# Optimization experiments

Measured on AMD Instinct MI355X. Metric: run time of the kernel, lower is better.

Reference implementation:

```python
import jax, jax.numpy as jnp
import numpy as np
import math

L, B, S, D, H, DI, V = 4, 2, 1024, 768, 12, 3072, 512
DK = D // H

def gelu_tanh(x):
    c = math.sqrt(2.0 / math.pi)
    return 0.5 * x * (1.0 + jnp.tanh(c * (x + 0.044715 * x ** 3)))

def layer_norm(x, g, b, eps=1e-5):
    mu = jnp.mean(x, axis=-1, keepdims=True)
    var = jnp.var(x, axis=-1, keepdims=True)
    return (x - mu) * jax.lax.rsqrt(var + eps) * g + b

def setup_inputs() -> dict:
    key = jax.random.key(0)
    ks = jax.random.split(key, 12)
    w = 0.02  # init scale
    return {
        "x": jax.random.randint(ks[0], (B, S), 0, V),
        "embed": jax.random.normal(ks[1], (V, D), jnp.float32) * w,
        "pos_emb": jax.random.normal(ks[2], (S, D), jnp.float32) * w,
        "ln1_g": jnp.ones((L, D), jnp.float32),
        "ln1_b": jnp.zeros((L, D), jnp.float32),
        "wq": jax.random.normal(ks[3], (L, D, D), jnp.float32) * w,
        "bq": jnp.zeros((L, D), jnp.float32),
        "wk": jax.random.normal(ks[4], (L, D, D), jnp.float32) * w,
        "bk": jnp.zeros((L, D), jnp.float32),
        "wv": jax.random.normal(ks[5], (L, D, D), jnp.float32) * w,
        "bv": jnp.zeros((L, D), jnp.float32),
        "wo": jax.random.normal(ks[6], (L, D, D), jnp.float32) * w,
        "bo": jnp.zeros((L, D), jnp.float32),
        "ln2_g": jnp.ones((L, D), jnp.float32),
        "ln2_b": jnp.zeros((L, D), jnp.float32),
        "w_in": jax.random.normal(ks[7], (L, D, DI), jnp.float32) * w,
        "b_in": jnp.zeros((L, DI), jnp.float32),
        "w_out": jax.random.normal(ks[8], (L, DI, D), jnp.float32) * w,
        "b_out": jnp.zeros((L, D), jnp.float32),
        "lnf_g": jnp.ones((D,), jnp.float32),
        "lnf_b": jnp.zeros((D,), jnp.float32),
        "out_w": jax.random.normal(ks[9], (D, V), jnp.float32) * w,
    }

def reference(x, embed, pos_emb, ln1_g, ln1_b, wq, bq, wk, bk, wv, bv, wo, bo,
              ln2_g, ln2_b, w_in, b_in, w_out, b_out, lnf_g, lnf_b, out_w):
    s = x.shape[1]
    h = embed[x] + pos_emb[None, :s]                       # [B,S,D]
    causal = jnp.tril(jnp.ones((s, s), bool))              # True = keep
    scale = 1.0 / math.sqrt(DK)
    for l in range(L):
        a = layer_norm(h, ln1_g[l], ln1_b[l])
        q = (a @ wq[l] + bq[l]).reshape(-1, s, H, DK)
        k = (a @ wk[l] + bk[l]).reshape(-1, s, H, DK)
        v = (a @ wv[l] + bv[l]).reshape(-1, s, H, DK)
        scores = jnp.einsum('bqhd,bkhd->bhqk', q, k) * scale
        scores = jnp.where(causal, scores, -jnp.inf)
        attn = jax.nn.softmax(scores, axis=-1)
        o = jnp.einsum('bhqk,bkhd->bqhd', attn, v).reshape(-1, s, D)
        h = h + o @ wo[l] + bo[l]
        f = layer_norm(h, ln2_g[l], ln2_b[l])
        h = h + gelu_tanh(f @ w_in[l] + b_in[l]) @ w_out[l] + b_out[l]
    h = layer_norm(h, lnf_g, lnf_b)
    return h @ out_w                                       # [B,S,V] logits
```

## Files before the change

kernel.cpp:

```cpp
#include <hip/hip_runtime.h>
#include <hip/hip_bf16.h>


#define TKN    2048
#define DMODEL 768
#define SEQ    1024
#define NH     12
#define DHEAD  64
#define DFF    3072
#define NL     4
#define NVOCAB 512
#define NQKV   2304

typedef unsigned short u16;
typedef __attribute__((ext_vector_type(4))) float f32x4;
typedef __attribute__((ext_vector_type(8))) short short8;
typedef __attribute__((ext_vector_type(4))) unsigned short us4;

__device__ __forceinline__ u16 f2bf(float f) {
  unsigned u = __builtin_bit_cast(unsigned, f);
  u += 0x7fffu + ((u >> 16) & 1u);
  return (u16)(u >> 16);
}

__device__ __forceinline__ short8 mk8(us4 lo, us4 hi) {
  short8 r;
  r[0] = (short)lo[0]; r[1] = (short)lo[1]; r[2] = (short)lo[2]; r[3] = (short)lo[3];
  r[4] = (short)hi[0]; r[5] = (short)hi[1]; r[6] = (short)hi[2]; r[7] = (short)hi[3];
  return r;
}

__device__ __forceinline__ void gload16(const u16* g, u16* l) {
  __builtin_amdgcn_global_load_lds(
      (const __attribute__((address_space(1))) unsigned int*)g,
      (__attribute__((address_space(3))) unsigned int*)l, 16, 0, 0);
}

__global__ __launch_bounds__(256) void k_embed(const int* __restrict__ x,
                                               const float* __restrict__ emb,
                                               const float* __restrict__ pos,
                                               float* __restrict__ h) {
  int t = blockIdx.x;
  int s = t & (SEQ - 1);
  int id = x[t];
  int d = threadIdx.x;
#pragma unroll
  for (int j = 0; j < 3; ++j, d += 256)
    h[t * DMODEL + d] = emb[id * DMODEL + d] + pos[s * DMODEL + d];
}

__global__ __launch_bounds__(256) void k_ln(const float* __restrict__ h,
                                            const float* __restrict__ gam,
                                            const float* __restrict__ bet,
                                            u16* __restrict__ out) {
  __shared__ float sbuf[8];
  int row = blockIdx.x, tid = threadIdx.x;
  const float* hr = h + (size_t)row * DMODEL;
  float x0 = hr[tid], x1 = hr[tid + 256], x2 = hr[tid + 512];
  float s = x0 + x1 + x2;
#pragma unroll
  for (int off = 32; off > 0; off >>= 1) s += __shfl_down(s, off);
  if ((tid & 63) == 0) sbuf[tid >> 6] = s;
  __syncthreads();
  float mu = (sbuf[0] + sbuf[1] + sbuf[2] + sbuf[3]) * (1.0f / DMODEL);
  float d0 = x0 - mu, d1 = x1 - mu, d2 = x2 - mu;
  float v = d0 * d0 + d1 * d1 + d2 * d2;
#pragma unroll
  for (int off = 32; off > 0; off >>= 1) v += __shfl_down(v, off);
  if ((tid & 63) == 0) sbuf[4 + (tid >> 6)] = v;
  __syncthreads();
  float var = (sbuf[4] + sbuf[5] + sbuf[6] + sbuf[7]) * (1.0f / DMODEL);
  float rstd = rsqrtf(var + 1e-5f);
  size_t o = (size_t)row * DMODEL;
  out[o + tid]       = f2bf(d0 * rstd * gam[tid]       + bet[tid]);
  out[o + tid + 256] = f2bf(d1 * rstd * gam[tid + 256] + bet[tid + 256]);
  out[o + tid + 512] = f2bf(d2 * rstd * gam[tid + 512] + bet[tid + 512]);
}

__device__ __forceinline__ void cvt_tile(const float* __restrict__ src, int ldS,
                                         int k0, int n0src,
                                         u16* __restrict__ dst, int ldD, int n0dst,
                                         int tid, u16 (*tl)[72]) {
  int kr = tid >> 2, nj = (tid & 3) << 4;
  const float* sp = src + (size_t)(k0 + kr) * ldS + n0src + nj;
  float4 a0 = ((const float4*)sp)[0];
  float4 a1 = ((const float4*)sp)[1];
  float4 a2 = ((const float4*)sp)[2];
  float4 a3 = ((const float4*)sp)[3];
  u16* tr = &tl[kr][nj];
  tr[0]=f2bf(a0.x); tr[1]=f2bf(a0.y); tr[2]=f2bf(a0.z); tr[3]=f2bf(a0.w);
  tr[4]=f2bf(a1.x); tr[5]=f2bf(a1.y); tr[6]=f2bf(a1.z); tr[7]=f2bf(a1.w);
  tr[8]=f2bf(a2.x); tr[9]=f2bf(a2.y); tr[10]=f2bf(a2.z); tr[11]=f2bf(a2.w);
  tr[12]=f2bf(a3.x); tr[13]=f2bf(a3.y); tr[14]=f2bf(a3.z); tr[15]=f2bf(a3.w);
  __syncthreads();
  int nr = tid >> 2, kj = (tid & 3) << 4;
  us4 o[4];
#pragma unroll
  for (int c = 0; c < 4; ++c)
#pragma unroll
    for (int i = 0; i < 4; ++i) o[c][i] = tl[kj + c * 4 + i][nr];
  u16* dp = dst + (size_t)(n0dst + nr) * ldD + k0 + kj;
  ((us4*)dp)[0] = o[0]; ((us4*)dp)[1] = o[1];
  ((us4*)dp)[2] = o[2]; ((us4*)dp)[3] = o[3];
}

__global__ __launch_bounds__(256) void k_cvtL(const float* __restrict__ wq,
                                              const float* __restrict__ wk,
                                              const float* __restrict__ wv,
                                              const float* __restrict__ wo,
                                              const float* __restrict__ win,
                                              const float* __restrict__ wout,
                                              u16* __restrict__ wqkvT,
                                              u16* __restrict__ woT,
                                              u16* __restrict__ winT,
                                              u16* __restrict__ woutT) {
  __shared__ u16 tl[64][72];
  int t = blockIdx.x, tid = threadIdx.x;
  if (t < 432) {
    int kt = t % 12, ntile = t / 12;
    int gn0 = ntile * 64, sel = gn0 / DMODEL;
    const float* src = sel == 0 ? wq : sel == 1 ? wk : wv;
    cvt_tile(src, DMODEL, kt * 64, gn0 - sel * DMODEL, wqkvT, DMODEL, gn0, tid, tl);
  } else if (t < 576) {
    int t2 = t - 432, kt = t2 % 12, nt = t2 / 12;
    cvt_tile(wo, DMODEL, kt * 64, nt * 64, woT, DMODEL, nt * 64, tid, tl);
  } else if (t < 1152) {
    int t3 = t - 576, kt = t3 % 12, nt = t3 / 12;
    cvt_tile(win, DFF, kt * 64, nt * 64, winT, DMODEL, nt * 64, tid, tl);
  } else {
    int t4 = t - 1152, kt = t4 % 48, nt = t4 / 48;
    cvt_tile(wout, DMODEL, kt * 64, nt * 64, woutT, DFF, nt * 64, tid, tl);
  }
}

__global__ __launch_bounds__(256) void k_cvtT(const float* __restrict__ src,
                                              u16* __restrict__ dst,
                                              int K, int N) {
  __shared__ u16 tl[64][72];
  cvt_tile(src, N, blockIdx.x * 64, blockIdx.y * 64, dst, K, blockIdx.y * 64,
           threadIdx.x, tl);
}

__global__ __launch_bounds__(256) void k_packb(const float* __restrict__ bq,
                                               const float* __restrict__ bk,
                                               const float* __restrict__ bv,
                                               float* __restrict__ dst) {
  int i = blockIdx.x * 256 + threadIdx.x;
  if (i < NL * NQKV) {
    int l = i / NQKV, j = i - l * NQKV;
    float v = j < DMODEL ? bq[l * DMODEL + j]
            : j < 2 * DMODEL ? bk[l * DMODEL + j - DMODEL]
            : bv[l * DMODEL + j - 2 * DMODEL];
    dst[i] = v;
  }
}

template <int EP, int BMv>
__global__ __launch_bounds__(256) void k_mm(const u16* __restrict__ A,
                                            const u16* __restrict__ BT,
                                            const float* __restrict__ bias,
                                            void* __restrict__ outp,
                                            int N, int K) {
  constexpr int MI = BMv / 32;
  __shared__ __align__(16) u16 As[2][BMv * 64];
  __shared__ __align__(16) u16 Bs[2][128 * 64];
  const int nbx = gridDim.x;
  int lin = blockIdx.y * nbx + blockIdx.x;
  const int chunk = (nbx * gridDim.y) >> 3;
  lin = (lin & 7) * chunk + (lin >> 3);
  const int bn = (lin % nbx) * 128, bm = (lin / nbx) * BMv;

  const int tid = threadIdx.x, lane = tid & 63, wid = tid >> 6;
  const int g = lane >> 4, fl = lane & 15;
  const int wm = wid >> 1, wn = wid & 1;

  const int srow = wid * 8 + (lane >> 3);
  const int scol = ((lane & 7) ^ (lane >> 3)) << 3;
  const u16* ag = A + (size_t)(bm + srow) * K + scol;
  const u16* bg = BT + (size_t)(bn + srow) * K + scol;

  f32x4 acc[MI][4] = {};
  const int sw = (fl & 7) << 4;

  auto stage = [&](int buf, int kk) {
#pragma unroll
    for (int is = 0; is < MI; ++is)
      gload16(ag + kk + (size_t)is * 32 * K, &As[buf][wid * 512 + is * 2048]);
#pragma unroll
    for (int is = 0; is < 4; ++is)
      gload16(bg + kk + (size_t)is * 32 * K, &Bs[buf][wid * 512 + is * 2048]);
  };

  const int nk = K >> 6;
  stage(0, 0);
  __syncthreads();
  int cur = 0;
  for (int kt = 0; kt < nk; ++kt) {
    if (kt + 1 < nk) stage(cur ^ 1, (kt + 1) << 6);
#pragma unroll
    for (int k0 = 0; k0 < 64; k0 += 32) {
      const int bo = (k0 + 4 * g) * 2;
      short8 af[MI], bf[4];
#pragma unroll
      for (int i = 0; i < MI; ++i) {
        const char* base = (const char*)&As[cur][(wm * (BMv / 2) + i * 16 + fl) * 64];
        af[i] = mk8(*(const us4*)(base + (bo ^ sw)),
                    *(const us4*)(base + ((bo + 32) ^ sw)));
      }
#pragma unroll
      for (int j = 0; j < 4; ++j) {
        const char* base = (const char*)&Bs[cur][(wn * 64 + j * 16 + fl) * 64];
        bf[j] = mk8(*(const us4*)(base + (bo ^ sw)),
                    *(const us4*)(base + ((bo + 32) ^ sw)));
      }
#pragma unroll
      for (int i = 0; i < MI; ++i)
#pragma unroll
        for (int j = 0; j < 4; ++j)
          acc[i][j] = __builtin_amdgcn_mfma_f32_16x16x32_bf16(af[i], bf[j], acc[i][j], 0, 0, 0);
    }
    __syncthreads();
    cur ^= 1;
  }

  const int row0 = bm + wm * (BMv / 2) + 4 * g;
  const int col0 = bn + wn * 64 + fl;
#pragma unroll
  for (int j = 0; j < 4; ++j) {
    int col = col0 + j * 16;
    float bv = (EP == 3) ? 0.0f : bias[col];
#pragma unroll
    for (int i = 0; i < MI; ++i) {
#pragma unroll
      for (int r = 0; r < 4; ++r) {
        int row = row0 + i * 16 + r;
        float val = acc[i][j][r] + bv;
        size_t idx = (size_t)row * N + col;
        if (EP == 0) {
          ((u16*)outp)[idx] = f2bf(val);
        } else if (EP == 1) {
          ((float*)outp)[idx] += val;
        } else if (EP == 2) {
          float t = 0.7978845608028654f * (val + 0.044715f * val * val * val);
          ((u16*)outp)[idx] = f2bf(0.5f * val * (1.0f + tanhf(t)));
        } else {
          ((float*)outp)[idx] = val;
        }
      }
    }
  }
}

__global__ __launch_bounds__(256) void k_attn(const u16* __restrict__ qkv,
                                              float* __restrict__ pO,
                                              float* __restrict__ pML) {
  __shared__ u16 Vt[2][DHEAD * 68];
  int lin = blockIdx.y * gridDim.x + blockIdx.x;
  const int chunk = (gridDim.x * gridDim.y) >> 3;
  lin = (lin & 7) * chunk + (lin >> 3);
  const int qb = lin % gridDim.x;
  const int bh = lin / gridDim.x;
  const int sp = blockIdx.z;
  const int b = bh / NH, hh = bh % NH;
  const int tid = threadIdx.x, lane = tid & 63, w = tid >> 6;
  const int g = lane >> 4, fl = lane & 15;
  const int qrow = qb * 64 + w * 16 + fl;
  const u16* qp = qkv + (size_t)(b * SEQ + qrow) * NQKV + hh * DHEAD;

  short8 qf[2];
#pragma unroll
  for (int hf = 0; hf < 2; ++hf) {
    us4 lo = *(const us4*)(qp + hf * 32 + 4 * g);
    us4 hi = *(const us4*)(qp + hf * 32 + 16 + 4 * g);
    qf[hf] = mk8(lo, hi);
  }

  float m = -1e30f, lsum = 0.0f;
  f32x4 oacc[4] = {};
  const int qmaxw = qb * 64 + w * 16 + 15;
  const int vr = tid >> 2, vd = (tid & 3) << 4;
  const u16* vbase = qkv + (size_t)(b * SEQ + vr) * NQKV + 2 * DMODEL + hh * DHEAD + vd;
  const u16* kbase0 = qkv + (size_t)(b * SEQ) * NQKV + DMODEL + hh * DHEAD;

  const int nt = qb + 1;
  const int t_lo = (sp * nt) >> 1, t_hi = ((sp + 1) * nt) >> 1;

  if (t_lo < t_hi) {
    {
      const u16* vp = vbase + (size_t)t_lo * 64 * NQKV;
      us4 vv[4];
#pragma unroll
      for (int qi = 0; qi < 4; ++qi) vv[qi] = *(const us4*)(vp + qi * 4);
#pragma unroll
      for (int qi = 0; qi < 4; ++qi)
#pragma unroll
        for (int i = 0; i < 4; ++i) Vt[0][(vd + qi * 4 + i) * 68 + vr] = vv[qi][i];
    }
    __syncthreads();
    int cur = 0;
    for (int t64 = t_lo; t64 < t_hi; ++t64) {
      const u16* kb64 = kbase0 + (size_t)t64 * 64 * NQKV;
      us4 kv[4][4];
#pragma unroll
      for (int q4 = 0; q4 < 4; ++q4) {
        const u16* kp = kb64 + (size_t)(q4 * 16 + fl) * NQKV;
#pragma unroll
        for (int j = 0; j < 4; ++j) kv[q4][j] = *(const us4*)(kp + j * 16 + 4 * g);
      }
      const bool pf = (t64 + 1 < t_hi);
      us4 vvn[4];
      if (pf) {
        const u16* vp = vbase + (size_t)(t64 + 1) * 64 * NQKV;
#pragma unroll
        for (int qi = 0; qi < 4; ++qi) vvn[qi] = *(const us4*)(vp + qi * 4);
      }

#pragma unroll
      for (int i32 = 0; i32 < 2; ++i32) {
        int kb = t64 * 64 + i32 * 32;
        if (kb <= qmaxw) {
          f32x4 sfr[2];
#pragma unroll
          for (int sub = 0; sub < 2; ++sub) {
            int q4 = i32 * 2 + sub;
            short8 kf0 = mk8(kv[q4][0], kv[q4][1]);
            short8 kf1 = mk8(kv[q4][2], kv[q4][3]);
            f32x4 s = {};
            s = __builtin_amdgcn_mfma_f32_16x16x32_bf16(kf0, qf[0], s, 0, 0, 0);
            s = __builtin_amdgcn_mfma_f32_16x16x32_bf16(kf1, qf[1], s, 0, 0, 0);
            sfr[sub] = s;
          }
          float sc[8];
#pragma unroll
          for (int sub = 0; sub < 2; ++sub)
#pragma unroll
            for (int r = 0; r < 4; ++r) {
              int key = kb + sub * 16 + 4 * g + r;
              float sv = sfr[sub][r] * 0.125f;
              sc[sub * 4 + r] = (key <= qrow) ? sv : -1e30f;
            }
          float pmax = sc[0];
#pragma unroll
          for (int e = 1; e < 8; ++e) pmax = fmaxf(pmax, sc[e]);
          pmax = fmaxf(pmax, __shfl_xor(pmax, 16));
          pmax = fmaxf(pmax, __shfl_xor(pmax, 32));
          if (__all(pmax <= m + 8.0f)) {
            float p[8], ps = 0.0f;
#pragma unroll
            for (int e = 0; e < 8; ++e) { p[e] = __expf(sc[e] - m); ps += p[e]; }
            ps += __shfl_xor(ps, 16);
            ps += __shfl_xor(ps, 32);
            lsum += ps;
            short8 pfr;
#pragma unroll
            for (int e = 0; e < 8; ++e) pfr[e] = (short)f2bf(p[e]);
#pragma unroll
            for (int nb = 0; nb < 4; ++nb) {
              const u16* vtp = &Vt[cur][(nb * 16 + fl) * 68 + i32 * 32 + 4 * g];
              short8 vf = mk8(*(const us4*)vtp, *(const us4*)(vtp + 16));
              oacc[nb] = __builtin_amdgcn_mfma_f32_16x16x32_bf16(pfr, vf, oacc[nb], 0, 0, 0);
            }
          } else {
            float mnew = fmaxf(m, pmax);
            float corr = __expf(m - mnew);
            float p[8], ps = 0.0f;
#pragma unroll
            for (int e = 0; e < 8; ++e) { p[e] = __expf(sc[e] - mnew); ps += p[e]; }
            ps += __shfl_xor(ps, 16);
            ps += __shfl_xor(ps, 32);
            lsum = lsum * corr + ps;
            m = mnew;
            float cr[4];
#pragma unroll
            for (int r = 0; r < 4; ++r) cr[r] = __shfl(corr, 4 * g + r);
#pragma unroll
            for (int nb = 0; nb < 4; ++nb)
#pragma unroll
              for (int r = 0; r < 4; ++r) oacc[nb][r] *= cr[r];
            short8 pfr;
#pragma unroll
            for (int e = 0; e < 8; ++e) pfr[e] = (short)f2bf(p[e]);
#pragma unroll
            for (int nb = 0; nb < 4; ++nb) {
              const u16* vtp = &Vt[cur][(nb * 16 + fl) * 68 + i32 * 32 + 4 * g];
              short8 vf = mk8(*(const us4*)vtp, *(const us4*)(vtp + 16));
              oacc[nb] = __builtin_amdgcn_mfma_f32_16x16x32_bf16(pfr, vf, oacc[nb], 0, 0, 0);
            }
          }
        }
      }
      if (pf) {
        __syncthreads();
#pragma unroll
        for (int qi = 0; qi < 4; ++qi)
#pragma unroll
          for (int i = 0; i < 4; ++i) Vt[cur ^ 1][(vd + qi * 4 + i) * 68 + vr] = vvn[qi][i];
        __syncthreads();
        cur ^= 1;
      }
    }
  }

  const size_t part = ((size_t)bh * 16 + qb) * 2 + sp;
  float* ob = pO + part * 4096;
  float* ml = pML + part * 128;
#pragma unroll
  for (int nb = 0; nb < 4; ++nb)
#pragma unroll
    for (int r = 0; r < 4; ++r)
      ob[(w * 16 + 4 * g + r) * 64 + nb * 16 + fl] = oacc[nb][r];
  if (g == 0) {
    ml[w * 16 + fl] = m;
    ml[64 + w * 16 + fl] = lsum;
  }
}

__global__ __launch_bounds__(256) void k_ared(const float* __restrict__ pO,
                                              const float* __restrict__ pML,
                                              u16* __restrict__ O) {
  __shared__ float w0s[64], w1s[64], iLs[64];
  const int qb = blockIdx.x, bh = blockIdx.y;
  const int b = bh / NH, hh = bh % NH;
  const int tid = threadIdx.x;
  const size_t p0 = ((size_t)bh * 16 + qb) * 2;
  if (tid < 64) {
    float m0 = pML[p0 * 128 + tid], l0 = pML[p0 * 128 + 64 + tid];
    float m1 = pML[(p0 + 1) * 128 + tid], l1 = pML[(p0 + 1) * 128 + 64 + tid];
    float M = fmaxf(m0, m1);
    float w0 = __expf(m0 - M), w1 = __expf(m1 - M);
    w0s[tid] = w0; w1s[tid] = w1;
    iLs[tid] = 1.0f / (l0 * w0 + l1 * w1);
  }
  __syncthreads();
  const float* O0 = pO + p0 * 4096;
  const float* O1 = pO + (p0 + 1) * 4096;
  for (int i = tid; i < 4096; i += 256) {
    int row = i >> 6, d = i & 63;
    float v = (O0[i] * w0s[row] + O1[i] * w1s[row]) * iLs[row];
    O[(size_t)(b * SEQ + qb * 64 + row) * DMODEL + hh * DHEAD + d] = f2bf(v);
  }
}

extern "C" void kernel_launch(void* const* d_in, const int* in_sizes, int n_in,
                              void* d_out, int out_size, void* d_ws, size_t ws_size,
                              hipStream_t stream) {
  const int*   x    = (const int*)d_in[0];
  const float* emb  = (const float*)d_in[1];
  const float* pos  = (const float*)d_in[2];
  const float* ln1g = (const float*)d_in[3];
  const float* ln1b = (const float*)d_in[4];
  const float* wq   = (const float*)d_in[5];
  const float* bq   = (const float*)d_in[6];
  const float* wk   = (const float*)d_in[7];
  const float* bk   = (const float*)d_in[8];
  const float* wv   = (const float*)d_in[9];
  const float* bv   = (const float*)d_in[10];
  const float* wo   = (const float*)d_in[11];
  const float* bo   = (const float*)d_in[12];
  const float* ln2g = (const float*)d_in[13];
  const float* ln2b = (const float*)d_in[14];
  const float* win  = (const float*)d_in[15];
  const float* bin  = (const float*)d_in[16];
  const float* wout = (const float*)d_in[17];
  const float* bout = (const float*)d_in[18];
  const float* lnfg = (const float*)d_in[19];
  const float* lnfb = (const float*)d_in[20];
  const float* outw = (const float*)d_in[21];

  char* w8 = (char*)d_ws;
  float* h    = (float*)(w8);
  u16* abuf   = (u16*)(w8 + 6291456);
  u16* qkv    = (u16*)(w8 + 9437184);
  u16* obuf   = (u16*)(w8 + 18874368);
  u16* ffbuf  = (u16*)(w8 + 9437184);
  u16* wqkvT  = (u16*)(w8 + 22020096);
  u16* woT    = (u16*)(w8 + 25559040);
  u16* winT   = (u16*)(w8 + 26738688);
  u16* woutT  = (u16*)(w8 + 31457280);
  u16* outwT  = (u16*)(w8 + 36175872);
  float* bqkv = (float*)(w8 + 36962304);
  float* pO   = (float*)(w8 + 36999168);
  float* pML  = (float*)(w8 + 49582080);

  k_embed<<<TKN, 256, 0, stream>>>(x, emb, pos, h);
  k_packb<<<36, 256, 0, stream>>>(bq, bk, bv, bqkv);
  k_cvtT<<<dim3(12, 8), 256, 0, stream>>>(outw, outwT, DMODEL, NVOCAB);

  for (int l = 0; l < NL; ++l) {
    k_cvtL<<<1728, 256, 0, stream>>>(
        wq + (size_t)l * DMODEL * DMODEL, wk + (size_t)l * DMODEL * DMODEL,
        wv + (size_t)l * DMODEL * DMODEL, wo + (size_t)l * DMODEL * DMODEL,
        win + (size_t)l * DMODEL * DFF, wout + (size_t)l * DFF * DMODEL,
        wqkvT, woT, winT, woutT);

    k_ln<<<TKN, 256, 0, stream>>>(h, ln1g + l * DMODEL, ln1b + l * DMODEL, abuf);
    k_mm<0, 128><<<dim3(NQKV / 128, TKN / 128), 256, 0, stream>>>(
        abuf, wqkvT, bqkv + l * NQKV, qkv, NQKV, DMODEL);
    k_attn<<<dim3(SEQ / 64, 2 * NH, 2), 256, 0, stream>>>(qkv, pO, pML);
    k_ared<<<dim3(SEQ / 64, 2 * NH), 256, 0, stream>>>(pO, pML, obuf);
    k_mm<1, 64><<<dim3(DMODEL / 128, TKN / 64), 256, 0, stream>>>(
        obuf, woT, bo + l * DMODEL, h, DMODEL, DMODEL);
    k_ln<<<TKN, 256, 0, stream>>>(h, ln2g + l * DMODEL, ln2b + l * DMODEL, abuf);
    k_mm<2, 128><<<dim3(DFF / 128, TKN / 128), 256, 0, stream>>>(
        abuf, winT, bin + l * DFF, ffbuf, DFF, DMODEL);
    k_mm<1, 64><<<dim3(DMODEL / 128, TKN / 64), 256, 0, stream>>>(
        ffbuf, woutT, bout + l * DMODEL, h, DMODEL, DFF);
  }

  k_ln<<<TKN, 256, 0, stream>>>(h, lnfg, lnfb, abuf);
  k_mm<3, 64><<<dim3(NVOCAB / 128, TKN / 64), 256, 0, stream>>>(
      abuf, outwT, nullptr, d_out, NVOCAB, DMODEL);
}
```

Before: 822.7 us.

## Add split-K with atomic accumulation and narrower GEMM tiles for more blocks

Makes the GEMM tile width a template parameter and adds split-K over gridDim.z. The residual-add projections now accumulate partial sums into h with atomicAdd, and only the z=0 slice adds the bias. All GEMMs switch to 64-wide N tiles, and the Wo and W_out projections split K 2 and 4 ways, so the grids have many more blocks to fill the CUs. The cost is float atomics on the residual, which make summation order nondeterministic, plus extra output traffic and lower reuse per tile.

```diff
diff --git a/kernel.cpp b/kernel.cpp
--- a/kernel.cpp
+++ b/kernel.cpp
@@ -155,20 +155,21 @@
   }
 }
 
-template <int EP, int BMv>
+template <int EP, int BM, int BN>
 __global__ __launch_bounds__(256) void k_mm(const u16* __restrict__ A,
                                             const u16* __restrict__ BT,
                                             const float* __restrict__ bias,
                                             void* __restrict__ outp,
                                             int N, int K) {
-  constexpr int MI = BMv / 32;
-  __shared__ __align__(16) u16 As[2][BMv * 64];
-  __shared__ __align__(16) u16 Bs[2][128 * 64];
+  constexpr int MI = BM / 32;
+  constexpr int NJ = BN / 32;
+  __shared__ __align__(16) u16 As[2][BM * 64];
+  __shared__ __align__(16) u16 Bs[2][BN * 64];
   const int nbx = gridDim.x;
   int lin = blockIdx.y * nbx + blockIdx.x;
   const int chunk = (nbx * gridDim.y) >> 3;
   lin = (lin & 7) * chunk + (lin >> 3);
-  const int bn = (lin % nbx) * 128, bm = (lin / nbx) * BMv;
+  const int bn = (lin % nbx) * BN, bm = (lin / nbx) * BM;
 
   const int tid = threadIdx.x, lane = tid & 63, wid = tid >> 6;
   const int g = lane >> 4, fl = lane & 15;
@@ -179,7 +180,7 @@
   const u16* ag = A + (size_t)(bm + srow) * K + scol;
   const u16* bg = BT + (size_t)(bn + srow) * K + scol;
 
-  f32x4 acc[MI][4] = {};
+  f32x4 acc[MI][NJ] = {};
   const int sw = (fl & 7) << 4;
 
   auto stage = [&](int buf, int kk) {
@@ -187,48 +188,51 @@
     for (int is = 0; is < MI; ++is)
       gload16(ag + kk + (size_t)is * 32 * K, &As[buf][wid * 512 + is * 2048]);
 #pragma unroll
-    for (int is = 0; is < 4; ++is)
+    for (int is = 0; is < NJ; ++is)
       gload16(bg + kk + (size_t)is * 32 * K, &Bs[buf][wid * 512 + is * 2048]);
   };
 
-  const int nk = K >> 6;
-  stage(0, 0);
+  const int ks = K / gridDim.z;
+  const int kb0 = blockIdx.z * ks;
+  const int nk = ks >> 6;
+  stage(0, kb0);
   __syncthreads();
   int cur = 0;
   for (int kt = 0; kt < nk; ++kt) {
-    if (kt + 1 < nk) stage(cur ^ 1, (kt + 1) << 6);
+    if (kt + 1 < nk) stage(cur ^ 1, kb0 + ((kt + 1) << 6));
 #pragma unroll
     for (int k0 = 0; k0 < 64; k0 += 32) {
       const int bo = (k0 + 4 * g) * 2;
-      short8 af[MI], bf[4];
+      short8 af[MI], bf[NJ];
 #pragma unroll
       for (int i = 0; i < MI; ++i) {
-        const char* base = (const char*)&As[cur][(wm * (BMv / 2) + i * 16 + fl) * 64];
+        const char* base = (const char*)&As[cur][(wm * (BM / 2) + i * 16 + fl) * 64];
         af[i] = mk8(*(const us4*)(base + (bo ^ sw)),
                     *(const us4*)(base + ((bo + 32) ^ sw)));
       }
 #pragma unroll
-      for (int j = 0; j < 4; ++j) {
-        const char* base = (const char*)&Bs[cur][(wn * 64 + j * 16 + fl) * 64];
+      for (int j = 0; j < NJ; ++j) {
+        const char* base = (const char*)&Bs[cur][(wn * (BN / 2) + j * 16 + fl) * 64];
         bf[j] = mk8(*(const us4*)(base + (bo ^ sw)),
                     *(const us4*)(base + ((bo + 32) ^ sw)));
       }
 #pragma unroll
       for (int i = 0; i < MI; ++i)
 #pragma unroll
-        for (int j = 0; j < 4; ++j)
+        for (int j = 0; j < NJ; ++j)
           acc[i][j] = __builtin_amdgcn_mfma_f32_16x16x32_bf16(af[i], bf[j], acc[i][j], 0, 0, 0);
     }
     __syncthreads();
     cur ^= 1;
   }
 
-  const int row0 = bm + wm * (BMv / 2) + 4 * g;
-  const int col0 = bn + wn * 64 + fl;
-#pragma unroll
-  for (int j = 0; j < 4; ++j) {
+  const int row0 = bm + wm * (BM / 2) + 4 * g;
+  const int col0 = bn + wn * (BN / 2) + fl;
+#pragma unroll
+  for (int j = 0; j < NJ; ++j) {
     int col = col0 + j * 16;
     float bv = (EP == 3) ? 0.0f : bias[col];
+    if (EP == 1 && blockIdx.z != 0) bv = 0.0f;
 #pragma unroll
     for (int i = 0; i < MI; ++i) {
 #pragma unroll
@@ -239,7 +243,7 @@
         if (EP == 0) {
           ((u16*)outp)[idx] = f2bf(val);
         } else if (EP == 1) {
-          ((float*)outp)[idx] += val;
+          atomicAdd(&((float*)outp)[idx], val);
         } else if (EP == 2) {
           float t = 0.7978845608028654f * (val + 0.044715f * val * val * val);
           ((u16*)outp)[idx] = f2bf(0.5f * val * (1.0f + tanhf(t)));
@@ -494,20 +498,20 @@
         wqkvT, woT, winT, woutT);
 
     k_ln<<<TKN, 256, 0, stream>>>(h, ln1g + l * DMODEL, ln1b + l * DMODEL, abuf);
-    k_mm<0, 128><<<dim3(NQKV / 128, TKN / 128), 256, 0, stream>>>(
+    k_mm<0, 128, 64><<<dim3(NQKV / 64, TKN / 128, 1), 256, 0, stream>>>(
         abuf, wqkvT, bqkv + l * NQKV, qkv, NQKV, DMODEL);
     k_attn<<<dim3(SEQ / 64, 2 * NH, 2), 256, 0, stream>>>(qkv, pO, pML);
     k_ared<<<dim3(SEQ / 64, 2 * NH), 256, 0, stream>>>(pO, pML, obuf);
-    k_mm<1, 64><<<dim3(DMODEL / 128, TKN / 64), 256, 0, stream>>>(
+    k_mm<1, 128, 64><<<dim3(DMODEL / 64, TKN / 128, 2), 256, 0, stream>>>(
         obuf, woT, bo + l * DMODEL, h, DMODEL, DMODEL);
     k_ln<<<TKN, 256, 0, stream>>>(h, ln2g + l * DMODEL, ln2b + l * DMODEL, abuf);
-    k_mm<2, 128><<<dim3(DFF / 128, TKN / 128), 256, 0, stream>>>(
+    k_mm<2, 128, 64><<<dim3(DFF / 64, TKN / 128, 1), 256, 0, stream>>>(
         abuf, winT, bin + l * DFF, ffbuf, DFF, DMODEL);
-    k_mm<1, 64><<<dim3(DMODEL / 128, TKN / 64), 256, 0, stream>>>(
+    k_mm<1, 128, 64><<<dim3(DMODEL / 64, TKN / 128, 4), 256, 0, stream>>>(
         ffbuf, woutT, bout + l * DMODEL, h, DMODEL, DFF);
   }
 
   k_ln<<<TKN, 256, 0, stream>>>(h, lnfg, lnfb, abuf);
-  k_mm<3, 64><<<dim3(NVOCAB / 128, TKN / 64), 256, 0, stream>>>(
+  k_mm<3, 64, 64><<<dim3(NVOCAB / 64, TKN / 64, 1), 256, 0, stream>>>(
       abuf, outwT, nullptr, d_out, NVOCAB, DMODEL);
 }
```

After: 709.8 us. 13.7% less time.
